# Performance work log

Measured on AMD Instinct MI355X. Metric: run time of the kernel, lower is better.

Reference implementation:

```python
import jax, jax.numpy as jnp
import numpy as np

T = 4.0          # kd_T
PATCH_NUM = 16
MASK_NUM = 4
P = PATCH_NUM - MASK_NUM  # 12
B = 4096
D_IN = 640
D = 128


def embed(x, w1, b1, w2, b2):
    # Linear -> ReLU -> Linear -> L2 normalize over features
    h = jax.nn.relu(x @ w1.T + b1)
    y = h @ w2.T + b2
    norm = jnp.sqrt(jnp.sum(y * y, axis=1, keepdims=True))
    return y / norm


def kl_rows(y_s, y_t):
    # Matches KLDiv: kl_div(log_softmax(y_s/T), softmax(y_t/T), 'batchmean') * T^2
    # over dim=0 of a 1-D vector -> sum / D. Vectorized over leading dims.
    ls = jax.nn.log_softmax(y_s / T, axis=-1)
    lt = jax.nn.log_softmax(y_t / T, axis=-1)
    pt = jnp.exp(lt)
    return jnp.sum(pt * (lt - ls), axis=-1) / y_s.shape[-1] * (T * T)


def setup_inputs() -> dict:
    key = jax.random.key(0)
    ks = jax.random.split(key, 11)
    return {
        "ebg": jax.random.normal(ks[0], (B, D_IN), jnp.float32),
        "ebp": jax.random.normal(ks[1], (P * B, D_IN), jnp.float32),
        "labelsg": jax.random.randint(ks[2], (B,), 0, 64),
        "glo_w1": jax.random.normal(ks[3], (D, D_IN), jnp.float32) * 0.04,
        "glo_b1": jax.random.normal(ks[4], (D,), jnp.float32) * 0.02,
        "glo_w2": jax.random.normal(ks[5], (D, D), jnp.float32) * 0.09,
        "glo_b2": jax.random.normal(ks[6], (D,), jnp.float32) * 0.02,
        "pat_w1": jax.random.normal(ks[7], (D, D_IN), jnp.float32) * 0.04,
        "pat_b1": jax.random.normal(ks[8], (D,), jnp.float32) * 0.02,
        "pat_w2": jax.random.normal(ks[9], (D, D), jnp.float32) * 0.09,
        "pat_b2": jax.random.normal(ks[10], (D,), jnp.float32) * 0.02,
    }


def reference(ebg, ebp, labelsg, glo_w1, glo_b1, glo_w2, glo_b2,
              pat_w1, pat_b1, pat_w2, pat_b2):
    sg = jax.lax.stop_gradient
    g = embed(ebg, glo_w1, glo_b1, glo_w2, glo_b2)          # [B, D]
    p = embed(ebp, pat_w1, pat_b1, pat_w2, pat_b2)          # [P*B, D]
    p = p.reshape(P, B, D)
    p_bar = p.mean(axis=0)                                  # [B, D]

    # soft_dil_loss: symmetric KL between g[b] and p_bar[b]
    dil = jnp.sum(kl_rows(g, sg(p_bar)) + kl_rows(p_bar, sg(g)))

    # soft_dcl_loss: symmetric KL between (g[b]-p[b,l])^2 and (p_bar[b]-p[b,l])^2
    p_bt = jnp.transpose(p, (1, 0, 2))                      # [B, P, D]
    d1 = (g[:, None, :] - p_bt) ** 2                        # [B, P, D]
    d2 = (p_bar[:, None, :] - p_bt) ** 2                    # [B, P, D]
    dcl = jnp.sum(kl_rows(d1, sg(d2)) + kl_rows(d2, sg(d1))) / P

    return (dil, dcl)
```

## Files before the change

### kernel.cpp

```cpp
#include <hip/hip_runtime.h>
#include <math.h>

#define B_    4096
#define DIN   640
#define DD    128
#define PP    12
#define INV_T 0.25f

typedef __bf16 bft;
typedef __attribute__((ext_vector_type(8))) __bf16 bf16x8;
typedef __attribute__((ext_vector_type(4))) float fx4;

__device__ __forceinline__ void gload16(const float* gp, float* lp) {
  __builtin_amdgcn_global_load_lds(
      (const __attribute__((address_space(1))) unsigned int*)gp,
      (__attribute__((address_space(3))) unsigned int*)lp,
      16, 0, 0);
}

__global__ __launch_bounds__(256) void prep_kernel(
    const float* __restrict__ gw1, const float* __restrict__ pw1,
    const float* __restrict__ gw2, const float* __restrict__ pw2,
    bft* __restrict__ w1hg, bft* __restrict__ w1lg,
    bft* __restrict__ w1hp, bft* __restrict__ w1lp,
    bft* __restrict__ w2hg, bft* __restrict__ w2lg,
    bft* __restrict__ w2hp, bft* __restrict__ w2lp)
{
  int idx = blockIdx.x * 256 + threadIdx.x;
  const float* src; bft *dh, *dl; int off;
  if (idx < 81920)       { src = gw1; dh = w1hg; dl = w1lg; off = idx; }
  else if (idx < 163840) { src = pw1; dh = w1hp; dl = w1lp; off = idx - 81920; }
  else if (idx < 180224) { src = gw2; dh = w2hg; dl = w2lg; off = idx - 163840; }
  else                   { src = pw2; dh = w2hp; dl = w2lp; off = idx - 180224; }
  float x = src[off];
  bft h = (bft)x;
  dh[off] = h;
  dl[off] = (bft)(x - (float)h);
}

__global__ __launch_bounds__(256, 2) void embed_kernel(
    const float* __restrict__ ebg, const float* __restrict__ ebp,
    const bft* __restrict__ w1hg, const bft* __restrict__ w1lg, const float* __restrict__ b1g,
    const bft* __restrict__ w2hg, const bft* __restrict__ w2lg, const float* __restrict__ b2g,
    const bft* __restrict__ w1hp, const bft* __restrict__ w1lp, const float* __restrict__ b1p,
    const bft* __restrict__ w2hp, const bft* __restrict__ w2lp, const float* __restrict__ b2p,
    float* __restrict__ outg, float* __restrict__ outp)
{
  __shared__ bft hsm[2 * 128 * 128];
  float* xb0 = (float*)hsm;
  float* xb1 = xb0 + 4096;
  bft* hhi = hsm;
  bft* hlo = hsm + 128 * 128;
  float* halfsq = (float*)hsm;

  const int t = threadIdx.x;
  const int w = t >> 6, lane = t & 63;
  const int wm = w >> 1, wn = w & 1;
  const int ln = lane & 15, quad = lane >> 4;

  const float *X, *B1, *B2;
  const bft *W1H, *W1L, *W2H, *W2L;
  float* Y;
  long m0;
  if (blockIdx.x < 32) {
    X = ebg; W1H = w1hg; W1L = w1lg; B1 = b1g; W2H = w2hg; W2L = w2lg; B2 = b2g;
    Y = outg; m0 = (long)blockIdx.x * 128;
  } else {
    X = ebp; W1H = w1hp; W1L = w1lp; B1 = b1p; W2H = w2hp; W2L = w2lp; B2 = b2p;
    Y = outp; m0 = (long)(blockIdx.x - 32) * 128;
  }

  const int srow = lane >> 3;
  const int skq  = (lane & 7) ^ srow;
  const float* xsrc = X + (size_t)(m0 + w * 32 + srow) * DIN + skq * 4;
  const int ldst = w * 32 * 32 + lane * 4;

#define GLX(bufp, k0)                                        \
  _Pragma("unroll")                                          \
  for (int j = 0; j < 4; j++)                                \
    gload16(xsrc + (size_t)j * 8 * DIN + (k0), (bufp) + ldst + j * 8 * 32);

  const int s0 = ((quad << 1) ^ (ln & 7));

  const bft *p1h[4], *p1l[4];
#pragma unroll
  for (int nt = 0; nt < 4; nt++) {
    int n = wn * 64 + nt * 16 + ln;
    p1h[nt] = W1H + (size_t)n * DIN + quad * 8;
    p1l[nt] = W1L + (size_t)n * DIN + quad * 8;
  }

  fx4 acc[4][4];
#pragma unroll
  for (int mt = 0; mt < 4; mt++)
#pragma unroll
    for (int nt = 0; nt < 4; nt++) acc[mt][nt] = (fx4){0.f, 0.f, 0.f, 0.f};

#define LOADW(wh, wl, koff)                                \
  _Pragma("unroll")                                        \
  for (int nt = 0; nt < 4; nt++) {                         \
    wh[nt] = *(const bf16x8*)(p1h[nt] + (koff));           \
    wl[nt] = *(const bf16x8*)(p1l[nt] + (koff));           \
  }

#define PH1CHUNK(bufp, wh, wl)                                                         \
  {                                                                                    \
    bf16x8 ah[4], al[4];                                                               \
    _Pragma("unroll")                                                                  \
    for (int mt = 0; mt < 4; mt++) {                                                   \
      const float* rp = (bufp) + (wm * 64 + mt * 16 + ln) * 32;                        \
      fx4 x0 = *(const fx4*)(rp + s0 * 4);                                             \
      fx4 x1 = *(const fx4*)(rp + (s0 ^ 1) * 4);                                       \
      _Pragma("unroll")                                                                \
      for (int j = 0; j < 4; j++) {                                                    \
        float xv = x0[j];                                                              \
        bft hh = (bft)xv;                                                              \
        ah[mt][j] = hh;                                                                \
        al[mt][j] = (bft)(xv - (float)hh);                                             \
        float yv = x1[j];                                                              \
        bft hh2 = (bft)yv;                                                             \
        ah[mt][4 + j] = hh2;                                                           \
        al[mt][4 + j] = (bft)(yv - (float)hh2);                                        \
      }                                                                                \
    }                                                                                  \
    _Pragma("unroll")                                                                  \
    for (int mt = 0; mt < 4; mt++)                                                     \
      _Pragma("unroll")                                                                \
      for (int nt = 0; nt < 4; nt++) {                                                 \
        acc[mt][nt] = __builtin_amdgcn_mfma_f32_16x16x32_bf16(ah[mt], wh[nt], acc[mt][nt], 0, 0, 0); \
        acc[mt][nt] = __builtin_amdgcn_mfma_f32_16x16x32_bf16(al[mt], wh[nt], acc[mt][nt], 0, 0, 0); \
        acc[mt][nt] = __builtin_amdgcn_mfma_f32_16x16x32_bf16(ah[mt], wl[nt], acc[mt][nt], 0, 0, 0); \
      }                                                                                \
  }

  bf16x8 wha[4], wla[4], whb[4], wlb[4];
  GLX(xb0, 0)
  LOADW(wha, wla, 0)
  __syncthreads();
  for (int kc = 0; kc < 20; kc += 2) {
    const int k0 = kc * 32;
    GLX(xb1, k0 + 32)
    LOADW(whb, wlb, k0 + 32)
    PH1CHUNK(xb0, wha, wla)
    __syncthreads();
    if (kc < 18) {
      GLX(xb0, k0 + 64)
      LOADW(wha, wla, k0 + 64)
    }
    PH1CHUNK(xb1, whb, wlb)
    __syncthreads();
  }

#pragma unroll
  for (int nt = 0; nt < 4; nt++) {
    float bv = B1[wn * 64 + nt * 16 + ln];
    int c8 = wn * 8 + nt * 2 + (ln >> 3);
    int c7 = ln & 7;
#pragma unroll
    for (int mt = 0; mt < 4; mt++) {
#pragma unroll
      for (int r = 0; r < 4; r++) {
        float v = fmaxf(acc[mt][nt][r] + bv, 0.f);
        bft h = (bft)v;
        bft l = (bft)(v - (float)h);
        int m = wm * 64 + mt * 16 + quad * 4 + r;
        int addr = m * 128 + ((c8 ^ (m & 15)) << 3) + c7;
        hhi[addr] = h;
        hlo[addr] = l;
      }
    }
  }

  const bft *p2h[4], *p2l[4];
#pragma unroll
  for (int nt = 0; nt < 4; nt++) {
    int n = wn * 64 + nt * 16 + ln;
    p2h[nt] = W2H + (size_t)n * DD + quad * 8;
    p2l[nt] = W2L + (size_t)n * DD + quad * 8;
  }
  fx4 acc2[4][4];
#pragma unroll
  for (int nt = 0; nt < 4; nt++) {
    float bv = B2[wn * 64 + nt * 16 + ln];
#pragma unroll
    for (int mt = 0; mt < 4; mt++) acc2[mt][nt] = (fx4){bv, bv, bv, bv};
  }

#define LOADW2(wh, wl, koff)                               \
  _Pragma("unroll")                                        \
  for (int nt = 0; nt < 4; nt++) {                         \
    wh[nt] = *(const bf16x8*)(p2h[nt] + (koff));           \
    wl[nt] = *(const bf16x8*)(p2l[nt] + (koff));           \
  }

#define PH2CHUNK(kcv, wh, wl)                                                          \
  {                                                                                    \
    bf16x8 ah2[4], al2[4];                                                             \
    _Pragma("unroll")                                                                  \
    for (int mt = 0; mt < 4; mt++) {                                                   \
      int m = wm * 64 + mt * 16 + ln;                                                  \
      int c8 = ((kcv) * 4 + quad) ^ (m & 15);                                          \
      ah2[mt] = *(const bf16x8*)&hhi[m * 128 + (c8 << 3)];                             \
      al2[mt] = *(const bf16x8*)&hlo[m * 128 + (c8 << 3)];                             \
    }                                                                                  \
    _Pragma("unroll")                                                                  \
    for (int mt = 0; mt < 4; mt++)                                                     \
      _Pragma("unroll")                                                                \
      for (int nt = 0; nt < 4; nt++) {                                                 \
        acc2[mt][nt] = __builtin_amdgcn_mfma_f32_16x16x32_bf16(ah2[mt], wh[nt], acc2[mt][nt], 0, 0, 0); \
        acc2[mt][nt] = __builtin_amdgcn_mfma_f32_16x16x32_bf16(al2[mt], wh[nt], acc2[mt][nt], 0, 0, 0); \
        acc2[mt][nt] = __builtin_amdgcn_mfma_f32_16x16x32_bf16(ah2[mt], wl[nt], acc2[mt][nt], 0, 0, 0); \
      }                                                                                \
  }

  bf16x8 q2ha[4], q2la[4], q2hb[4], q2lb[4];
  LOADW2(q2ha, q2la, 0)
  __syncthreads();
  LOADW2(q2hb, q2lb, 32)
  PH2CHUNK(0, q2ha, q2la)
  LOADW2(q2ha, q2la, 64)
  PH2CHUNK(1, q2hb, q2lb)
  LOADW2(q2hb, q2lb, 96)
  PH2CHUNK(2, q2ha, q2la)
  PH2CHUNK(3, q2hb, q2lb)
  __syncthreads();

#pragma unroll
  for (int mt = 0; mt < 4; mt++) {
#pragma unroll
    for (int r = 0; r < 4; r++) {
      float s = 0.f;
#pragma unroll
      for (int nt = 0; nt < 4; nt++) { float v = acc2[mt][nt][r]; s += v * v; }
      s += __shfl_xor(s, 1, 64);
      s += __shfl_xor(s, 2, 64);
      s += __shfl_xor(s, 4, 64);
      s += __shfl_xor(s, 8, 64);
      if (ln == 0) halfsq[(wm * 64 + mt * 16 + quad * 4 + r) * 2 + wn] = s;
    }
  }
  __syncthreads();
#pragma unroll
  for (int mt = 0; mt < 4; mt++) {
#pragma unroll
    for (int r = 0; r < 4; r++) {
      int row = wm * 64 + mt * 16 + quad * 4 + r;
      float rinv = 1.0f / sqrtf(halfsq[row * 2] + halfsq[row * 2 + 1]);
#pragma unroll
      for (int nt = 0; nt < 4; nt++)
        Y[(m0 + row) * DD + wn * 64 + nt * 16 + ln] = acc2[mt][nt][r] * rinv;
    }
  }
}

__device__ __forceinline__ float sym_kl_row(float au0, float au1, float av0, float av1)
{
  float eu0 = __expf(au0), eu1 = __expf(au1);
  float ev0 = __expf(av0), ev1 = __expf(av1);
  float su = eu0 + eu1, sv = ev0 + ev1;
#pragma unroll
  for (int o = 32; o > 0; o >>= 1) {
    su += __shfl_xor(su, o, 64);
    sv += __shfl_xor(sv, o, 64);
  }
  float ru = 1.0f / su, rv = 1.0f / sv;
  float d0 = au0 - av0, d1 = au1 - av1;
  float part = (eu0 * ru - ev0 * rv) * d0 + (eu1 * ru - ev1 * rv) * d1;
#pragma unroll
  for (int o = 32; o > 0; o >>= 1) part += __shfl_xor(part, o, 64);
  return part;
}

__global__ __launch_bounds__(256) void loss_kernel(
    const float* __restrict__ g, const float* __restrict__ p,
    float* __restrict__ pdil, float* __restrict__ pdcl)
{
  __shared__ float wd[4], wc[4];
  int w = threadIdx.x >> 6, lane = threadIdx.x & 63;
  int b = blockIdx.x * 4 + w;
  float2 pl[PP];
  float sx = 0.f, sy = 0.f;
#pragma unroll
  for (int l = 0; l < PP; l++) {
    pl[l] = *(const float2*)&p[((size_t)l * B_ + b) * DD + lane * 2];
    sx += pl[l].x; sy += pl[l].y;
  }
  sx *= (1.0f / PP); sy *= (1.0f / PP);
  float2 gv = *(const float2*)&g[(size_t)b * DD + lane * 2];

  float dil = sym_kl_row(gv.x * INV_T, gv.y * INV_T, sx * INV_T, sy * INV_T) * 0.125f;

  float dcl = 0.f;
#pragma unroll
  for (int l = 0; l < PP; l++) {
    float u0 = (gv.x - pl[l].x) * (gv.x - pl[l].x) * INV_T;
    float u1 = (gv.y - pl[l].y) * (gv.y - pl[l].y) * INV_T;
    float v0 = (sx - pl[l].x) * (sx - pl[l].x) * INV_T;
    float v1 = (sy - pl[l].y) * (sy - pl[l].y) * INV_T;
    dcl += sym_kl_row(u0, u1, v0, v1);
  }
  dcl *= (1.0f / 96.0f);

  if (lane == 0) { wd[w] = dil; wc[w] = dcl; }
  __syncthreads();
  if (threadIdx.x == 0) pdil[blockIdx.x] = wd[0] + wd[1] + wd[2] + wd[3];
  if (threadIdx.x == 1) pdcl[blockIdx.x] = wc[0] + wc[1] + wc[2] + wc[3];
}

__global__ __launch_bounds__(256) void final_kernel(const float* __restrict__ pdil,
                                                    const float* __restrict__ pdcl,
                                                    float* __restrict__ out)
{
  __shared__ float red[8];
  int t = threadIdx.x;
  float s0 = 0.f, s1 = 0.f;
  for (int i = t; i < 1024; i += 256) { s0 += pdil[i]; s1 += pdcl[i]; }
#pragma unroll
  for (int o = 32; o > 0; o >>= 1) {
    s0 += __shfl_xor(s0, o, 64);
    s1 += __shfl_xor(s1, o, 64);
  }
  int wid = t >> 6, lane = t & 63;
  if (lane == 0) { red[wid] = s0; red[4 + wid] = s1; }
  __syncthreads();
  if (t == 0) out[0] = red[0] + red[1] + red[2] + red[3];
  if (t == 1) out[1] = red[4] + red[5] + red[6] + red[7];
}

extern "C" void kernel_launch(void* const* d_in, const int* in_sizes, int n_in,
                              void* d_out, int out_size, void* d_ws, size_t ws_size,
                              hipStream_t stream)
{
  const float* ebg = (const float*)d_in[0];
  const float* ebp = (const float*)d_in[1];
  const float* gw1 = (const float*)d_in[3];
  const float* gb1 = (const float*)d_in[4];
  const float* gw2 = (const float*)d_in[5];
  const float* gb2 = (const float*)d_in[6];
  const float* pw1 = (const float*)d_in[7];
  const float* pb1 = (const float*)d_in[8];
  const float* pw2 = (const float*)d_in[9];
  const float* pb2 = (const float*)d_in[10];
  float* out = (float*)d_out;

  float* ws   = (float*)d_ws;
  float* g    = ws;
  float* p    = g + (size_t)B_ * DD;
  float* pdil = p + (size_t)PP * B_ * DD;
  float* pdcl = pdil + 1024;
  bft* wb     = (bft*)(pdcl + 1024);
  bft* w1hg = wb;                 bft* w1lg = w1hg + 81920;
  bft* w1hp = w1lg + 81920;       bft* w1lp = w1hp + 81920;
  bft* w2hg = w1lp + 81920;       bft* w2lg = w2hg + 16384;
  bft* w2hp = w2lg + 16384;       bft* w2lp = w2hp + 16384;

  prep_kernel<<<768, 256, 0, stream>>>(gw1, pw1, gw2, pw2,
                                       w1hg, w1lg, w1hp, w1lp,
                                       w2hg, w2lg, w2hp, w2lp);
  embed_kernel<<<416, 256, 0, stream>>>(ebg, ebp,
                                        w1hg, w1lg, gb1, w2hg, w2lg, gb2,
                                        w1hp, w1lp, pb1, w2hp, w2lp, pb2,
                                        g, p);
  loss_kernel<<<B_ / 4, 256, 0, stream>>>(g, p, pdil, pdcl);
  final_kernel<<<1, 256, 0, stream>>>(pdil, pdcl, out);
}
```

Measured before the change: 268.0 us.

## Use four-slot LDS ring with prefetch depth three and one barrier per chunk

Replaces the double-buffered X staging in the first GEMM with a 4-slot LDS ring. Three chunks are prefetched ahead, and each step waits with an explicit s_waitcnt vmcnt count instead of a full __syncthreads, so there is one barrier per chunk instead of two. The aim is to hide global load latency better and cut synchronization stalls. It relies on hand-tuned vmcnt constants and issues dummy loads at the tail, which risks correctness if the counts do not match.

```diff
diff --git a/kernel.cpp b/kernel.cpp
--- a/kernel.cpp
+++ b/kernel.cpp
@@ -47,8 +47,7 @@
     float* __restrict__ outg, float* __restrict__ outp)
 {
   __shared__ bft hsm[2 * 128 * 128];
-  float* xb0 = (float*)hsm;
-  float* xb1 = xb0 + 4096;
+  float* xbase = (float*)hsm;
   bft* hhi = hsm;
   bft* hlo = hsm + 128 * 128;
   float* halfsq = (float*)hsm;
@@ -134,22 +133,32 @@
   }
 
   bf16x8 wha[4], wla[4], whb[4], wlb[4];
-  GLX(xb0, 0)
+  GLX(xbase, 0)
+  GLX(xbase + 4096, 32)
+  GLX(xbase + 8192, 64)
   LOADW(wha, wla, 0)
-  __syncthreads();
-  for (int kc = 0; kc < 20; kc += 2) {
-    const int k0 = kc * 32;
-    GLX(xb1, k0 + 32)
-    LOADW(whb, wlb, k0 + 32)
-    PH1CHUNK(xb0, wha, wla)
-    __syncthreads();
-    if (kc < 18) {
-      GLX(xb0, k0 + 64)
-      LOADW(wha, wla, k0 + 64)
-    }
-    PH1CHUNK(xb1, whb, wlb)
-    __syncthreads();
-  }
+
+#define HALFSTEP(c, WCH, WCL, WNH, WNL, VMTOK)                              \
+  {                                                                          \
+    const int kn_ = ((c) + 1 < 20) ? ((c) + 1) * 32 : 0;                     \
+    LOADW(WNH, WNL, kn_)                                                     \
+    asm volatile("s_waitcnt vmcnt(" VMTOK ") lgkmcnt(0)" ::: "memory");      \
+    __builtin_amdgcn_s_barrier();                                            \
+    __builtin_amdgcn_sched_barrier(0);                                       \
+    const int kp_ = ((c) + 3 < 20) ? ((c) + 3) * 32 : 0;                     \
+    float* pslot_ = xbase + ((((c) + 3) & 3) << 12);                         \
+    GLX(pslot_, kp_)                                                         \
+    PH1CHUNK(xbase + ((((c) & 3)) << 12), WCH, WCL)                          \
+  }
+
+  HALFSTEP(0, wha, wla, whb, wlb, "24")
+  for (int kc = 1; kc < 19; kc += 2) {
+    HALFSTEP(kc,     whb, wlb, wha, wla, "32")
+    HALFSTEP(kc + 1, wha, wla, whb, wlb, "32")
+  }
+  HALFSTEP(19, whb, wlb, wha, wla, "32")
+
+  __syncthreads();
 
 #pragma unroll
   for (int nt = 0; nt < 4; nt++) {
```

Result: no change. 265.1 us (-1.1%).
